# Performance work log

Measured on AMD Instinct MI355X. Metric: run time of the kernel, lower is better.

## Reference

```python
import jax, jax.numpy as jnp
import numpy as np

E = 1024          # embed_dim
T = 32 * 32 + 1   # spacial_dim^2 + 1 (cls-like mean token)
H = 16            # num_heads = E // 64
CH = E // H       # per-head channels


def setup_inputs() -> dict:
    key = jax.random.key(0)
    k1, k2, k3, k4 = jax.random.split(key, 4)
    x = jax.random.normal(k1, (16, E, T - 1), dtype=jnp.float32)
    pos_emb = jax.random.normal(k2, (E, T), dtype=jnp.float32) / (E ** 0.5)
    w_qkv = jax.random.normal(k3, (3 * E, E), dtype=jnp.float32) * (E ** -0.5)
    b_qkv = jnp.zeros((3 * E,), dtype=jnp.float32)
    w_c = jax.random.normal(k4, (E, E), dtype=jnp.float32) * (E ** -0.5)
    b_c = jnp.zeros((E,), dtype=jnp.float32)
    return {"x": x, "pos_emb": pos_emb, "w_qkv": w_qkv, "b_qkv": b_qkv,
            "w_c": w_c, "b_c": b_c}


def reference(x, pos_emb, w_qkv, b_qkv, w_c, b_c):
    b, c, _ = x.shape
    # prepend mean token, add positional embedding
    x = jnp.concatenate([x.mean(axis=-1, keepdims=True), x], axis=-1)  # [b, E, T]
    x = x + pos_emb[None].astype(x.dtype)
    # 1x1 conv == channel matmul: [b, 3E, T]
    qkv = jnp.einsum('oc,bct->bot', w_qkv, x) + b_qkv[None, :, None]
    t = qkv.shape[-1]
    q, k, v = jnp.split(qkv, 3, axis=1)               # each [b, H*CH, T]
    q = q.reshape(b * H, CH, t)
    k = k.reshape(b * H, CH, t)
    v = v.reshape(b * H, CH, t)
    scale = 1.0 / (CH ** 0.25)
    w = jnp.einsum('bct,bcs->bts', q * scale, k * scale)  # [b*H, T, T]
    w = jax.nn.softmax(w.astype(jnp.float32), axis=-1).astype(qkv.dtype)
    a = jnp.einsum('bts,bcs->bct', w, v)              # [b*H, CH, T]
    a = a.reshape(b, H * CH, t)
    out = jnp.einsum('oc,bct->bot', w_c, a) + b_c[None, :, None]
    return out[:, :, 0]                               # [b, out_dim]
```

## Files before the change

### kernel.cpp

```cpp
#include <hip/hip_runtime.h>

#define B 16
#define E 1024
#define T 1025
#define SP 1024
#define H 16
#define ESTR 516

#define OFF_X0    0
#define OFF_U     (OFF_X0 + B*E)
#define OFF_PT    (OFF_U + B*H*E)
#define OFF_P0    (OFF_PT + B*SP*H)
#define OFF_A     (OFF_P0 + 1024)
#define OFF_POSA  (OFF_A + B*E)
#define OFF_SCP   (OFF_POSA + E*SP)
#define OFF_YP    (OFF_SCP + 32*256*SP)

__device__ __forceinline__ float blockReduceSum(float v, float* sm) {
    int tid = threadIdx.x;
    sm[tid] = v; __syncthreads();
    for (int s = 128; s > 0; s >>= 1) {
        if (tid < s) sm[tid] += sm[tid + s];
        __syncthreads();
    }
    float r = sm[0]; __syncthreads();
    return r;
}

__device__ __forceinline__ float blockReduceMax(float v, float* sm) {
    int tid = threadIdx.x;
    sm[tid] = v; __syncthreads();
    for (int s = 128; s > 0; s >>= 1) {
        if (tid < s) sm[tid] = fmaxf(sm[tid], sm[tid + s]);
        __syncthreads();
    }
    float r = sm[0]; __syncthreads();
    return r;
}

__device__ __forceinline__ float reduce16x64(const float v[16], int lane) {
    float r8[8], r4[4], r2[2], r1;
    {
        int bit = lane & 1;
        #pragma unroll
        for (int j = 0; j < 8; ++j) {
            float mine  = bit ? v[2*j+1] : v[2*j];
            float other = bit ? v[2*j]   : v[2*j+1];
            r8[j] = mine + __shfl_xor(other, 1, 64);
        }
    }
    {
        int bit = (lane >> 1) & 1;
        #pragma unroll
        for (int j = 0; j < 4; ++j) {
            float mine  = bit ? r8[2*j+1] : r8[2*j];
            float other = bit ? r8[2*j]   : r8[2*j+1];
            r4[j] = mine + __shfl_xor(other, 2, 64);
        }
    }
    {
        int bit = (lane >> 2) & 1;
        #pragma unroll
        for (int j = 0; j < 2; ++j) {
            float mine  = bit ? r4[2*j+1] : r4[2*j];
            float other = bit ? r4[2*j]   : r4[2*j+1];
            r2[j] = mine + __shfl_xor(other, 4, 64);
        }
    }
    {
        int bit = (lane >> 3) & 1;
        float mine  = bit ? r2[1] : r2[0];
        float other = bit ? r2[0] : r2[1];
        r1 = mine + __shfl_xor(other, 8, 64);
    }
    r1 += __shfl_xor(r1, 16, 64);
    r1 += __shfl_xor(r1, 32, 64);
    return r1;
}

__device__ __forceinline__ void gemv16(const float* __restrict__ wrow,
                                       const float* __restrict__ xin,
                                       float acc[16], int lane) {
    #pragma unroll
    for (int it = 0; it < 4; ++it) {
        int e4 = (it * 64 + lane) * 4;
        float4 wv = *(const float4*)(wrow + e4);
        #pragma unroll
        for (int b = 0; b < 16; ++b) {
            float4 xv = *(const float4*)(xin + (size_t)b * E + e4);
            acc[b] += wv.x * xv.x + wv.y * xv.y + wv.z * xv.z + wv.w * xv.w;
        }
    }
}

__global__ void k_pre(const float* __restrict__ x, const float* __restrict__ pos,
                      float* __restrict__ x0, float* __restrict__ posA) {
    int bid = blockIdx.x;
    int tid = threadIdx.x;
    if (bid < 4096) {
        int wave = tid >> 6, lane = tid & 63;
        int row = bid * 4 + wave;
        int e = row & (E - 1);
        const float4* x4 = (const float4*)(x + (size_t)row * SP);
        float s = 0.f;
        #pragma unroll
        for (int it = 0; it < 4; ++it) {
            float4 v = x4[it * 64 + lane];
            s += v.x + v.y + v.z + v.w;
        }
        #pragma unroll
        for (int m = 1; m < 64; m <<= 1) s += __shfl_xor(s, m, 64);
        if (lane == 0) x0[row] = s * (1.0f / SP) + pos[(size_t)e * T];
    } else {
        int e = bid - 4096;
        int t = tid * 4;
        const float* src = pos + (size_t)e * T + 1 + t;
        float4 v; v.x = src[0]; v.y = src[1]; v.z = src[2]; v.w = src[3];
        *(float4*)(posA + (size_t)e * SP + t) = v;
    }
}

__global__ void k_qu(const float* __restrict__ wqkv, const float* __restrict__ bqkv,
                     const float* __restrict__ x0, float* __restrict__ u) {
    int gid = blockIdx.x;
    int b = gid >> 4, h = gid & 15;
    int tid = threadIdx.x;
    int wave = tid >> 6, lane = tid & 63;
    __shared__ float xs0[1024 + 64];
    float* qs = xs0 + 1024;
    float4 x4v = *(const float4*)(x0 + (size_t)b * E + tid * 4);
    *(float4*)&xs0[tid * 4] = x4v;
    __syncthreads();
    float accs[16];
    #pragma unroll
    for (int i = 0; i < 16; ++i) accs[i] = 0.f;
    const float* wq = wqkv + (size_t)(h * 64 + wave * 16) * E;
    #pragma unroll
    for (int i = 0; i < 16; ++i) {
        const float* wr = wq + (size_t)i * E;
        float s = 0.f;
        #pragma unroll
        for (int k = 0; k < 4; ++k) {
            int e4 = (k * 64 + lane) * 4;
            float4 wv = *(const float4*)(wr + e4);
            float4 xv = *(const float4*)&xs0[e4];
            s += wv.x * xv.x + wv.y * xv.y + wv.z * xv.z + wv.w * xv.w;
        }
        accs[i] = s;
    }
    float tot = reduce16x64(accs, lane);
    if (lane < 16) qs[wave * 16 + lane] = tot + bqkv[h * 64 + wave * 16 + lane];
    __syncthreads();
    float4 acc = make_float4(0.f, 0.f, 0.f, 0.f);
    const float* wbase = wqkv + (size_t)(E + h * 64) * E + tid * 4;
    for (int c = 0; c < 64; ++c) {
        float4 wv = *(const float4*)(wbase + (size_t)c * E);
        float qv = qs[c];
        acc.x += qv * wv.x; acc.y += qv * wv.y;
        acc.z += qv * wv.z; acc.w += qv * wv.w;
    }
    *(float4*)(u + (size_t)gid * E + tid * 4) =
        make_float4(0.125f * acc.x, 0.125f * acc.y, 0.125f * acc.z, 0.125f * acc.w);
}

__global__ void __launch_bounds__(256, 2) k_scores(
        const float* __restrict__ x, const float* __restrict__ posA,
        const float* __restrict__ u, float* __restrict__ scp) {
    int gid = blockIdx.x;
    int es = gid >> 4;
    int b  = gid & 15;
    int e0 = es * 32;
    int tid = threadIdx.x;
    int t4 = tid * 4;
    __shared__ float us[H * 32];
    #pragma unroll
    for (int k = 0; k < 2; ++k) {
        int i = k * 256 + tid;
        int h = i >> 5, el = i & 31;
        us[h * 32 + el] = u[(size_t)(b * H + h) * E + e0 + el];
    }
    __syncthreads();
    float4 acc[H];
    #pragma unroll
    for (int h = 0; h < H; ++h) acc[h] = make_float4(0.f, 0.f, 0.f, 0.f);
    for (int eq = 0; eq < 8; ++eq) {
        float4 val[4];
        #pragma unroll
        for (int j = 0; j < 4; ++j) {
            int e = e0 + eq * 4 + j;
            float4 xv = *(const float4*)(x + ((size_t)(b * E + e)) * SP + t4);
            float4 pv = *(const float4*)(posA + (size_t)e * SP + t4);
            val[j] = make_float4(xv.x + pv.x, xv.y + pv.y, xv.z + pv.z, xv.w + pv.w);
        }
        #pragma unroll
        for (int h = 0; h < H; ++h) {
            float4 uu = *(const float4*)&us[h * 32 + eq * 4];
            acc[h].x += uu.x * val[0].x + uu.y * val[1].x + uu.z * val[2].x + uu.w * val[3].x;
            acc[h].y += uu.x * val[0].y + uu.y * val[1].y + uu.z * val[2].y + uu.w * val[3].y;
            acc[h].z += uu.x * val[0].z + uu.y * val[1].z + uu.z * val[2].z + uu.w * val[3].z;
            acc[h].w += uu.x * val[0].w + uu.y * val[1].w + uu.z * val[2].w + uu.w * val[3].w;
        }
    }
    #pragma unroll
    for (int h = 0; h < H; ++h)
        *(float4*)(scp + ((size_t)(es * 256) + b * H + h) * SP + t4) = acc[h];
}

__global__ void k_softmax(const float* __restrict__ u, const float* __restrict__ x0,
                          const float* __restrict__ scp, float* __restrict__ pT,
                          float* __restrict__ p0) {
    int bh = blockIdx.x;
    int b = bh >> 4, h = bh & 15;
    int tid = threadIdx.x;
    int t4 = tid * 4;
    __shared__ float sm[256];
    float4 uv = *(const float4*)(u + (size_t)bh * E + t4);
    float4 xv = *(const float4*)(x0 + (size_t)b * E + t4);
    float d = uv.x * xv.x + uv.y * xv.y + uv.z * xv.z + uv.w * xv.w;
    float s0 = blockReduceSum(d, sm);
    float4 v = make_float4(0.f, 0.f, 0.f, 0.f);
    #pragma unroll
    for (int es = 0; es < 32; ++es) {
        float4 pv = *(const float4*)(scp + ((size_t)(es * 256) + bh) * SP + t4);
        v.x += pv.x; v.y += pv.y; v.z += pv.z; v.w += pv.w;
    }
    float mx = fmaxf(fmaxf(v.x, v.y), fmaxf(v.z, v.w));
    mx = fmaxf(mx, s0);
    mx = blockReduceMax(mx, sm);
    v.x = expf(v.x - mx); v.y = expf(v.y - mx);
    v.z = expf(v.z - mx); v.w = expf(v.w - mx);
    float es0 = expf(s0 - mx);
    float sum = v.x + v.y + v.z + v.w + (tid == 0 ? es0 : 0.f);
    sum = blockReduceSum(sum, sm);
    float inv = 1.0f / sum;
    pT[((size_t)b * SP + t4 + 0) * H + h] = v.x * inv;
    pT[((size_t)b * SP + t4 + 1) * H + h] = v.y * inv;
    pT[((size_t)b * SP + t4 + 2) * H + h] = v.z * inv;
    pT[((size_t)b * SP + t4 + 3) * H + h] = v.w * inv;
    if (tid == 0) p0[bh] = es0 * inv;
}

__global__ void __launch_bounds__(256, 2) k_y(
        const float* __restrict__ x, const float* __restrict__ posA,
        const float* __restrict__ pT, float* __restrict__ yp) {
    int ts = blockIdx.x;
    int eh = blockIdx.y;
    int b  = blockIdx.z;
    int tid = threadIdx.x;
    int wave = tid >> 6, lane = tid & 63;
    int e0 = eh * 512;
    __shared__ float xs[16 * ESTR];
    __shared__ float psl[16][16];
    float acc[4][8];
    #pragma unroll
    for (int j = 0; j < 4; ++j)
        #pragma unroll
        for (int i = 0; i < 8; ++i) acc[j][i] = 0.f;

    for (int ch = 0; ch < 4; ++ch) {
        int t0 = ts * 64 + ch * 16;
        __syncthreads();
        #pragma unroll
        for (int i = 0; i < 8; ++i) {
            int f4id = i * 256 + tid;
            int row = f4id >> 2;
            int c4  = (f4id & 3) * 4;
            float4 xv = *(const float4*)(x + ((size_t)(b * E + e0 + row)) * SP + t0 + c4);
            float4 pv = *(const float4*)(posA + (size_t)(e0 + row) * SP + t0 + c4);
            xs[(c4 + 0) * ESTR + row] = xv.x + pv.x;
            xs[(c4 + 1) * ESTR + row] = xv.y + pv.y;
            xs[(c4 + 2) * ESTR + row] = xv.z + pv.z;
            xs[(c4 + 3) * ESTR + row] = xv.w + pv.w;
        }
        if (tid < 64) {
            int t = tid >> 2, hq = (tid & 3) * 4;
            float4 pv = *(const float4*)(pT + ((size_t)b * SP + t0 + t) * H + hq);
            psl[t][hq + 0] = pv.x; psl[t][hq + 1] = pv.y;
            psl[t][hq + 2] = pv.z; psl[t][hq + 3] = pv.w;
        }
        __syncthreads();
        #pragma unroll 4
        for (int t = 0; t < 16; ++t) {
            float4 xa = *(const float4*)&xs[t * ESTR + 4 * lane];
            float4 xb = *(const float4*)&xs[t * ESTR + 256 + 4 * lane];
            float4 pq = *(const float4*)&psl[t][4 * wave];
            float xch[8] = {xa.x, xa.y, xa.z, xa.w, xb.x, xb.y, xb.z, xb.w};
            float pch[4] = {pq.x, pq.y, pq.z, pq.w};
            #pragma unroll
            for (int j = 0; j < 4; ++j)
                #pragma unroll
                for (int i = 0; i < 8; ++i)
                    acc[j][i] += pch[j] * xch[i];
        }
    }
    #pragma unroll
    for (int j = 0; j < 4; ++j) {
        float* ypp = yp + (((size_t)ts * B + b) * H + 4 * wave + j) * E + e0;
        *(float4*)(ypp + 4 * lane) = make_float4(acc[j][0], acc[j][1], acc[j][2], acc[j][3]);
        *(float4*)(ypp + 256 + 4 * lane) = make_float4(acc[j][4], acc[j][5], acc[j][6], acc[j][7]);
    }
}

__global__ void k_yred_a(const float* __restrict__ yp, const float* __restrict__ p0,
                         const float* __restrict__ x0, const float* __restrict__ wqkv,
                         const float* __restrict__ bqkv, float* __restrict__ a) {
    int bh = blockIdx.x;
    int b = bh >> 4, h = bh & 15;
    int tid = threadIdx.x;
    int wave = tid >> 6, lane = tid & 63;
    __shared__ float ys[1024];
    int t4 = tid * 4;
    float p0v = p0[bh];
    float4 xv = *(const float4*)(x0 + (size_t)b * E + t4);
    float4 s = make_float4(p0v * xv.x, p0v * xv.y, p0v * xv.z, p0v * xv.w);
    #pragma unroll
    for (int ts = 0; ts < 16; ++ts) {
        float4 v = *(const float4*)(yp + ((size_t)(ts * 256) + bh) * E + t4);
        s.x += v.x; s.y += v.y; s.z += v.z; s.w += v.w;
    }
    *(float4*)&ys[t4] = s;
    __syncthreads();
    float xch[16];
    #pragma unroll
    for (int k = 0; k < 4; ++k) {
        float4 v = *(const float4*)&ys[lane * 16 + k * 4];
        xch[4*k+0] = v.x; xch[4*k+1] = v.y; xch[4*k+2] = v.z; xch[4*k+3] = v.w;
    }
    float accs[16];
    #pragma unroll
    for (int i = 0; i < 16; ++i) accs[i] = 0.f;
    #pragma unroll
    for (int i = 0; i < 16; ++i) {
        const float* wr = wqkv + (size_t)(2 * E + h * 64 + wave * 16 + i) * E + lane * 16;
        #pragma unroll
        for (int k = 0; k < 4; ++k) {
            float4 wv = *(const float4*)(wr + k * 4);
            accs[i] += wv.x * xch[4*k+0] + wv.y * xch[4*k+1]
                     + wv.z * xch[4*k+2] + wv.w * xch[4*k+3];
        }
    }
    float tot = reduce16x64(accs, lane);
    if (lane < 16) {
        int c = h * 64 + wave * 16 + lane;
        a[(size_t)b * E + c] = tot + bqkv[2 * E + c];
    }
}

__global__ void k_out(const float* __restrict__ wc, const float* __restrict__ bc,
                      const float* __restrict__ a, float* __restrict__ out) {
    int wave = threadIdx.x >> 6, lane = threadIdx.x & 63;
    int o = blockIdx.x * 4 + wave;
    float acc[16];
    #pragma unroll
    for (int b = 0; b < 16; ++b) acc[b] = 0.f;
    gemv16(wc + (size_t)o * E, a, acc, lane);
    float tot = reduce16x64(acc, lane);
    if (lane < 16) out[lane * E + o] = tot + bc[o];
}

extern "C" void kernel_launch(void* const* d_in, const int* in_sizes, int n_in,
                              void* d_out, int out_size, void* d_ws, size_t ws_size,
                              hipStream_t stream) {
    const float* x    = (const float*)d_in[0];
    const float* pos  = (const float*)d_in[1];
    const float* wqkv = (const float*)d_in[2];
    const float* bqkv = (const float*)d_in[3];
    const float* wc   = (const float*)d_in[4];
    const float* bc   = (const float*)d_in[5];
    float* out = (float*)d_out;
    float* ws  = (float*)d_ws;

    float* x0   = ws + OFF_X0;
    float* u    = ws + OFF_U;
    float* pT   = ws + OFF_PT;
    float* p0   = ws + OFF_P0;
    float* a    = ws + OFF_A;
    float* posA = ws + OFF_POSA;
    float* scp  = ws + OFF_SCP;
    float* yp   = ws + OFF_YP;

    k_pre<<<5120, 256, 0, stream>>>(x, pos, x0, posA);
    k_qu<<<256, 256, 0, stream>>>(wqkv, bqkv, x0, u);
    k_scores<<<512, 256, 0, stream>>>(x, posA, u, scp);
    k_softmax<<<256, 256, 0, stream>>>(u, x0, scp, pT, p0);
    k_y<<<dim3(16, 2, B), 256, 0, stream>>>(x, posA, pT, yp);
    k_yred_a<<<256, 256, 0, stream>>>(yp, p0, x0, wqkv, bqkv, a);
    k_out<<<256, 256, 0, stream>>>(wc, bc, a, out);
}
```

Before: 104.5 us.

## Split q/u projection into batched q0 GEMV and batch-shared K-weight kernel

The fused per-(batch,head) kernel, which re-read the Q and K weight slices once per batch, is replaced by two kernels. The first computes q0 for all 16 batches with a shared GEMV over the Q rows. The second multiplies each K-weight element by 8 batch queries held in shared memory, so each weight load is reused across batches. This cuts weight traffic by roughly the batch count, at the cost of one extra launch and a round trip of q0 through global memory.

```diff
diff --git a/kernel.cpp b/kernel.cpp
--- a/kernel.cpp
+++ b/kernel.cpp
@@ -8,7 +8,8 @@
 #define ESTR 516
 
 #define OFF_X0    0
-#define OFF_U     (OFF_X0 + B*E)
+#define OFF_Q0    (OFF_X0 + B*E)
+#define OFF_U     (OFF_Q0 + B*E)
 #define OFF_PT    (OFF_U + B*H*E)
 #define OFF_P0    (OFF_PT + B*SP*H)
 #define OFF_A     (OFF_P0 + 1024)
@@ -120,47 +121,45 @@
     }
 }
 
-__global__ void k_qu(const float* __restrict__ wqkv, const float* __restrict__ bqkv,
-                     const float* __restrict__ x0, float* __restrict__ u) {
-    int gid = blockIdx.x;
-    int b = gid >> 4, h = gid & 15;
-    int tid = threadIdx.x;
-    int wave = tid >> 6, lane = tid & 63;
-    __shared__ float xs0[1024 + 64];
-    float* qs = xs0 + 1024;
-    float4 x4v = *(const float4*)(x0 + (size_t)b * E + tid * 4);
-    *(float4*)&xs0[tid * 4] = x4v;
+__global__ void k_q0(const float* __restrict__ wqkv, const float* __restrict__ bqkv,
+                     const float* __restrict__ x0, float* __restrict__ q0) {
+    int wave = threadIdx.x >> 6, lane = threadIdx.x & 63;
+    int o = blockIdx.x * 4 + wave;
+    float acc[16];
+    #pragma unroll
+    for (int b = 0; b < 16; ++b) acc[b] = 0.f;
+    gemv16(wqkv + (size_t)o * E, x0, acc, lane);
+    float tot = reduce16x64(acc, lane);
+    if (lane < 16) q0[lane * E + o] = tot + bqkv[o];
+}
+
+__global__ void k_u(const float* __restrict__ wqkv, const float* __restrict__ q0,
+                    float* __restrict__ u) {
+    int ec = blockIdx.x;
+    int h  = blockIdx.y;
+    int tid = threadIdx.x;
+    __shared__ float qs[B * 64];
+    {
+        int b = tid >> 4, c4 = (tid & 15) * 4;
+        float4 v = *(const float4*)(q0 + (size_t)b * E + h * 64 + c4);
+        *(float4*)&qs[b * 64 + c4] = v;
+    }
     __syncthreads();
-    float accs[16];
-    #pragma unroll
-    for (int i = 0; i < 16; ++i) accs[i] = 0.f;
-    const float* wq = wqkv + (size_t)(h * 64 + wave * 16) * E;
-    #pragma unroll
-    for (int i = 0; i < 16; ++i) {
-        const float* wr = wq + (size_t)i * E;
-        float s = 0.f;
-        #pragma unroll
-        for (int k = 0; k < 4; ++k) {
-            int e4 = (k * 64 + lane) * 4;
-            float4 wv = *(const float4*)(wr + e4);
-            float4 xv = *(const float4*)&xs0[e4];
-            s += wv.x * xv.x + wv.y * xv.y + wv.z * xv.z + wv.w * xv.w;
-        }
-        accs[i] = s;
-    }
-    float tot = reduce16x64(accs, lane);
-    if (lane < 16) qs[wave * 16 + lane] = tot + bqkv[h * 64 + wave * 16 + lane];
-    __syncthreads();
-    float4 acc = make_float4(0.f, 0.f, 0.f, 0.f);
-    const float* wbase = wqkv + (size_t)(E + h * 64) * E + tid * 4;
+    int e  = ec * 128 + (tid & 127);
+    int bg = tid >> 7;
+    float acc[8];
+    #pragma unroll
+    for (int j = 0; j < 8; ++j) acc[j] = 0.f;
+    const float* wk = wqkv + (size_t)(E + h * 64) * E + e;
     for (int c = 0; c < 64; ++c) {
-        float4 wv = *(const float4*)(wbase + (size_t)c * E);
-        float qv = qs[c];
-        acc.x += qv * wv.x; acc.y += qv * wv.y;
-        acc.z += qv * wv.z; acc.w += qv * wv.w;
-    }
-    *(float4*)(u + (size_t)gid * E + tid * 4) =
-        make_float4(0.125f * acc.x, 0.125f * acc.y, 0.125f * acc.z, 0.125f * acc.w);
+        float wv = wk[(size_t)c * E];
+        #pragma unroll
+        for (int j = 0; j < 8; ++j)
+            acc[j] += wv * qs[(bg * 8 + j) * 64 + c];
+    }
+    #pragma unroll
+    for (int j = 0; j < 8; ++j)
+        u[((size_t)(bg * 8 + j) * H + h) * E + e] = 0.125f * acc[j];
 }
 
 __global__ void __launch_bounds__(256, 2) k_scores(
@@ -371,6 +370,7 @@
     float* ws  = (float*)d_ws;
 
     float* x0   = ws + OFF_X0;
+    float* q0   = ws + OFF_Q0;
     float* u    = ws + OFF_U;
     float* pT   = ws + OFF_PT;
     float* p0   = ws + OFF_P0;
@@ -380,7 +380,8 @@
     float* yp   = ws + OFF_YP;
 
     k_pre<<<5120, 256, 0, stream>>>(x, pos, x0, posA);
-    k_qu<<<256, 256, 0, stream>>>(wqkv, bqkv, x0, u);
+    k_q0<<<256, 256, 0, stream>>>(wqkv, bqkv, x0, q0);
+    k_u<<<dim3(8, 16), 256, 0, stream>>>(wqkv, q0, u);
     k_scores<<<512, 256, 0, stream>>>(x, posA, u, scp);
     k_softmax<<<256, 256, 0, stream>>>(u, x0, scp, pT, p0);
     k_y<<<dim3(16, 2, B), 256, 0, stream>>>(x, posA, pT, yp);
```

New measurement: 115.2 us. 10.3% more time.
